# Performance work log

Measured on AMD Instinct MI355X. Metric: run time of the kernel, lower is better.

## Reference

```python
import jax, jax.numpy as jnp
import numpy as np

B, M, S, N, DIN, C = 2048, 5, 128, 128, 64, 32
MID = C // 2  # 16
EPS = 1e-5
NEG_SLOPE = 0.2


def setup_inputs() -> dict:
    key = jax.random.key(0)
    ks = jax.random.split(key, 13)
    sc = lambda fan: 1.0 / np.sqrt(fan)
    return {
        "x_global": jax.random.normal(ks[0], (B, N, C), jnp.float32),
        "x_local": jax.random.normal(ks[1], (B * M, S, DIN), jnp.float32),
        "W_lin": jax.random.normal(ks[2], (C, DIN), jnp.float32) * sc(DIN),
        "b_lin": jnp.zeros((C,), jnp.float32),
        "W_att": jax.random.normal(ks[3], (C,), jnp.float32) * sc(C),  # Conv2d(C,1,1) weight
        "Wa": jax.random.normal(ks[4], (MID, C), jnp.float32) * sc(C),
        "Wb": jax.random.normal(ks[5], (MID, C), jnp.float32) * sc(C),
        "Wc": jax.random.normal(ks[6], (MID, C), jnp.float32) * sc(C),
        "Wn": jax.random.normal(ks[7], (MID, MID), jnp.float32) * sc(MID),
        "Wl": jax.random.normal(ks[8], (MID, MID), jnp.float32) * sc(MID),
        "Wd": jax.random.normal(ks[9], (C, 2 * MID), jnp.float32) * sc(2 * MID),
        "bn_gamma": jnp.ones((C,), jnp.float32),
        "bn_beta": jnp.zeros((C,), jnp.float32),
    }


def reference(x_global, x_local, W_lin, b_lin, W_att, Wa, Wb, Wc, Wn, Wl, Wd, bn_gamma, bn_beta):
    # --- Motion_Aggregation_Module.forward ---
    xl = x_local.reshape(B, M, S, DIN)
    xl = jnp.einsum('bmsd,cd->bmsc', xl, W_lin) + b_lin          # Linear(64,32)
    curves = jnp.transpose(xl, (0, 3, 1, 2))                      # [B,C,M,S]
    x = jnp.transpose(x_global, (0, 2, 1))                        # [B,C,N]

    # --- Correlation_Module.forward ---
    att = jnp.einsum('c,bcms->bms', W_att, curves)                # line_conv_att -> [B,M,S]
    inter = jnp.einsum('bcms,bms->bcm', curves, jax.nn.softmax(att, axis=-1))  # [B,C,M]
    intra = jnp.einsum('bcms,bms->bcs', curves, jax.nn.softmax(att, axis=-2))  # [B,C,S]

    inter = jnp.einsum('oc,bcm->bom', Wa, inter)                  # conva -> [B,MID,M]
    intra = jnp.einsum('oc,bcs->bos', Wb, intra)                  # convb -> [B,MID,S]
    x_logits = jnp.einsum('oc,bcn->bno', Wc, x)                   # convc^T -> [B,N,MID]

    a_inter = jax.nn.softmax(jnp.einsum('bno,bom->bnm', x_logits, inter), axis=-1)  # [B,N,M]
    a_intra = jax.nn.softmax(jnp.einsum('bno,bos->bns', x_logits, intra), axis=-1)  # [B,N,S]

    v_inter = jnp.einsum('po,bom->bmp', Wn, inter)                # convn^T -> [B,M,MID]
    v_intra = jnp.einsum('po,bos->bsp', Wl, intra)                # convl^T -> [B,S,MID]

    f_inter = jnp.einsum('bnm,bmp->bnp', a_inter, v_inter)        # [B,N,MID]
    f_intra = jnp.einsum('bns,bsp->bnp', a_intra, v_intra)        # [B,N,MID]
    feat = jnp.concatenate([f_inter, f_intra], axis=-1)           # [B,N,2*MID]
    feat = jnp.einsum('oc,bnc->bon', Wd, feat)                    # convd conv -> [B,C,N]

    # BatchNorm1d (training mode: batch stats over (B, N), biased variance)
    mean = feat.mean(axis=(0, 2), keepdims=True)
    var = feat.var(axis=(0, 2), keepdims=True)
    feat = (feat - mean) * jax.lax.rsqrt(var + EPS)
    feat = feat * bn_gamma[None, :, None] + bn_beta[None, :, None]

    out = x + feat                                                # residual
    out = jnp.where(out >= 0, out, NEG_SLOPE * out)               # leaky_relu(0.2)
    return jnp.transpose(out, (0, 2, 1))                          # [B,N,C]
```

## Files before the change

### kernel.cpp

```cpp
#include <hip/hip_runtime.h>
#include <math.h>

#define NB 2048
typedef float f32x4 __attribute__((ext_vector_type(4)));

#define P_WAL 0
#define P_WBL 1024
#define P_WLBL 2048
#define P_WNAL 3072
#define P_WEFF 4096
#define P_BWA 4160
#define P_BWB 4176
#define P_BWL 4192
#define P_BWN 4208
#define P_C0  4224

#define WS_BNPART 4352
#define WS_COEF   135424
#define WS_SMALL  135488
#define WS_BIG_I  463168
#define WS_BIG_V  (463168 + 4194304)

#define BSTAGE(MASK, HALF)                                        \
  { const bool hi_ = (lane & (MASK)) != 0;                        \
    _Pragma("unroll")                                             \
    for (int k_ = 0; k_ < (HALF); ++k_) {                         \
      float mine_ = hi_ ? a[k_ + (HALF)] : a[k_];                 \
      float oth_  = hi_ ? a[k_] : a[k_ + (HALF)];                 \
      a[k_] = mine_ + __shfl_xor(oth_, (MASK));                   \
    } }

__global__ __launch_bounds__(256) void k0_pre(const float* __restrict__ W_lin,
                                              const float* __restrict__ b_lin,
                                              const float* __restrict__ W_att,
                                              const float* __restrict__ Wa,
                                              const float* __restrict__ Wb,
                                              const float* __restrict__ Wn,
                                              const float* __restrict__ Wl,
                                              float* __restrict__ pre) {
  int t = threadIdx.x;
  for (int i = t; i < 1024; i += 256) {
    int o = i >> 6, d = i & 63;
    float sa = 0.f, sb = 0.f;
    for (int c = 0; c < 32; ++c) {
      float wl = W_lin[c * 64 + d];
      sa += Wa[o * 32 + c] * wl;
      sb += Wb[o * 32 + c] * wl;
    }
    pre[P_WAL + i] = sa;
    pre[P_WBL + i] = sb;
  }
  if (t < 64) {
    float s = 0.f;
    for (int c = 0; c < 32; ++c) s += W_att[c] * W_lin[c * 64 + t];
    pre[P_WEFF + t] = s;
  }
  if (t < 16) {
    float sa = 0.f, sb = 0.f;
    for (int c = 0; c < 32; ++c) {
      sa += Wa[t * 32 + c] * b_lin[c];
      sb += Wb[t * 32 + c] * b_lin[c];
    }
    pre[P_BWA + t] = sa;
    pre[P_BWB + t] = sb;
  }
  if (t == 0) {
    float s = 0.f;
    for (int c = 0; c < 32; ++c) s += W_att[c] * b_lin[c];
    pre[P_C0] = s;
  }
  __syncthreads();
  for (int i = t; i < 1024; i += 256) {
    int p_ = i >> 6, d = i & 63;
    float sl = 0.f, sn = 0.f;
    for (int o = 0; o < 16; ++o) {
      sl += Wl[p_ * 16 + o] * pre[P_WBL + o * 64 + d];
      sn += Wn[p_ * 16 + o] * pre[P_WAL + o * 64 + d];
    }
    pre[P_WLBL + i] = sl;
    pre[P_WNAL + i] = sn;
  }
  if (t < 16) {
    float sl = 0.f, sn = 0.f;
    for (int o = 0; o < 16; ++o) {
      sl += Wl[t * 16 + o] * pre[P_BWB + o];
      sn += Wn[t * 16 + o] * pre[P_BWA + o];
    }
    pre[P_BWL + t] = sl;
    pre[P_BWN + t] = sn;
  }
}

__global__ __launch_bounds__(512, 1) void k1a(
    const float* __restrict__ xl_all, const float* __restrict__ pre,
    float* __restrict__ p_small, float* __restrict__ bigI,
    float* __restrict__ bigV) {
  __shared__ __align__(16) float xaggi[128 * 68];
  __shared__ f32x4 scratch5[5][8][16];
  __shared__ float pe[5][8];
  __shared__ float xagg_inter[5][64];

  const int t = threadIdx.x;
  const int b = blockIdx.x;
  const int lane = t & 63;
  const int w = t >> 6;
  const int q = lane >> 4;
  const int i16 = lane & 15;

  const float* xl = xl_all + (size_t)b * (5 * 128 * 64);
  const f32x4 weff4 = ((const f32x4*)(pre + P_WEFF))[i16];
  const float c0 = pre[P_C0];

  const float* xb = xl + (size_t)(16 * w + q) * 64 + 4 * i16;

  f32x4 xA[4], xB[4], acc[4];
  float Zk[4];
  #pragma unroll
  for (int k = 0; k < 4; ++k) {
    acc[k] = (f32x4)0.f;
    Zk[k] = 0.f;
    xA[k] = *(const f32x4*)(xb + k * 256);
  }

  #pragma unroll
  for (int m = 0; m < 5; ++m) {
    f32x4* xc = (m & 1) ? xB : xA;
    f32x4* xn = (m & 1) ? xA : xB;
    if (m < 4) {
      const float* np = xb + (size_t)(m + 1) * 8192;
      #pragma unroll
      for (int k = 0; k < 4; ++k) xn[k] = *(const f32x4*)(np + k * 256);
    }
    float a0, a1, a2, a3;
    {
      f32x4 p0 = xc[0] * weff4, p1 = xc[1] * weff4, p2 = xc[2] * weff4, p3 = xc[3] * weff4;
      a0 = p0.x + p0.y + p0.z + p0.w;
      a1 = p1.x + p1.y + p1.z + p1.w;
      a2 = p2.x + p2.y + p2.z + p2.w;
      a3 = p3.x + p3.y + p3.z + p3.w;
    }
    #pragma unroll
    for (int mask = 1; mask <= 8; mask <<= 1) {
      a0 += __shfl_xor(a0, mask);
      a1 += __shfl_xor(a1, mask);
      a2 += __shfl_xor(a2, mask);
      a3 += __shfl_xor(a3, mask);
    }
    float e0 = __expf(a0 + c0), e1 = __expf(a1 + c0);
    float e2 = __expf(a2 + c0), e3 = __expf(a3 + c0);
    Zk[0] += e0; Zk[1] += e1; Zk[2] += e2; Zk[3] += e3;
    f32x4 pim;
    {
      f32x4 pr0 = e0 * xc[0];
      f32x4 pr1 = e1 * xc[1];
      f32x4 pr2 = e2 * xc[2];
      f32x4 pr3 = e3 * xc[3];
      acc[0] += pr0; acc[1] += pr1; acc[2] += pr2; acc[3] += pr3;
      pim = pr0 + pr1 + pr2 + pr3;
    }
    float se = e0 + e1 + e2 + e3;
    #pragma unroll
    for (int mask = 16; mask <= 32; mask <<= 1) {
      pim.x += __shfl_xor(pim.x, mask);
      pim.y += __shfl_xor(pim.y, mask);
      pim.z += __shfl_xor(pim.z, mask);
      pim.w += __shfl_xor(pim.w, mask);
      se += __shfl_xor(se, mask);
    }
    if (lane < 16) {
      scratch5[m][w][i16] = pim;
      if (i16 == 0) pe[m][w] = se;
    }
  }

  #pragma unroll
  for (int k = 0; k < 4; ++k) {
    float invz = 1.f / Zk[k];
    f32x4 v = acc[k] * invz;
    int r = 16 * w + 4 * k + q;
    *(f32x4*)&xaggi[r * 68 + 4 * i16] = v;
  }
  __syncthreads();

  if (t < 320) {
    int mm = t >> 6, d = t & 63;
    const float* sp = (const float*)&scratch5[mm][0][0];
    float s = 0.f;
    #pragma unroll
    for (int j = 0; j < 8; ++j) s += sp[j * 64 + d];
    float sume = pe[mm][0] + pe[mm][1] + pe[mm][2] + pe[mm][3] +
                 pe[mm][4] + pe[mm][5] + pe[mm][6] + pe[mm][7];
    xagg_inter[mm][d] = s / sume;
  }
  __syncthreads();

  {
    const int q2 = __builtin_amdgcn_readfirstlane(t >> 7);
    const int s2 = t & 127;
    const float* Wbase = pre + ((q2 < 2) ? P_WBL : P_WLBL) + (q2 & 1) * 512;
    const float* xrow = &xaggi[s2 * 68];
    float acc2[8];
    #pragma unroll
    for (int r = 0; r < 8; ++r) acc2[r] = 0.f;
    #pragma unroll
    for (int c = 0; c < 64; c += 4) {
      f32x4 xa = *(const f32x4*)(xrow + c);
      #pragma unroll
      for (int r = 0; r < 8; ++r)
        acc2[r] += xa.x * Wbase[r * 64 + c] + xa.y * Wbase[r * 64 + c + 1] +
                   xa.z * Wbase[r * 64 + c + 2] + xa.w * Wbase[r * 64 + c + 3];
    }
    const int bb = ((q2 < 2) ? P_BWB : P_BWL) + (q2 & 1) * 8;
    float* dst = ((q2 < 2) ? bigI : bigV) + (size_t)b * 2048 + s2 * 16 + (q2 & 1) * 8;
    f32x4 o0, o1;
    o0.x = acc2[0] + pre[bb + 0];
    o0.y = acc2[1] + pre[bb + 1];
    o0.z = acc2[2] + pre[bb + 2];
    o0.w = acc2[3] + pre[bb + 3];
    o1.x = acc2[4] + pre[bb + 4];
    o1.y = acc2[5] + pre[bb + 5];
    o1.z = acc2[6] + pre[bb + 6];
    o1.w = acc2[7] + pre[bb + 7];
    *(f32x4*)dst = o0;
    *(f32x4*)(dst + 4) = o1;
  }

  if (t < 160) {
    int o2 = t & 31, mm = t >> 5;
    const float* wr = pre + ((o2 < 16) ? (P_WAL + o2 * 64) : (P_WNAL + (o2 - 16) * 64));
    float p = 0.f;
    #pragma unroll
    for (int d = 0; d < 64; ++d) p += wr[d] * xagg_inter[mm][d];
    p += (o2 < 16) ? pre[P_BWA + o2] : pre[P_BWN + (o2 - 16)];
    float* os = p_small + (size_t)b * 160;
    if (o2 < 16) os[mm * 16 + o2] = p;
    else os[80 + mm * 16 + (o2 - 16)] = p;
  }
}

__global__ __launch_bounds__(128, 1) void k1b(
    const float* __restrict__ xg_all, const float* __restrict__ Wc_g,
    const float* __restrict__ Wd_g, const float* __restrict__ p_small,
    const float* __restrict__ bigI, const float* __restrict__ bigV,
    float* __restrict__ out, float* __restrict__ bn_part) {
  __shared__ f32x4 slabI[128][4];
  __shared__ f32x4 slabV[128][4];
  __shared__ float part1[2][32];
  __shared__ float part2[2][32];

  const int t = threadIdx.x;
  const int b = blockIdx.x;
  const int lane = t & 63;
  const int w = t >> 6;
  const int kmap = ((lane & 1) << 4) | ((lane & 2) << 2) | (lane & 4) |
                   ((lane >> 2) & 2) | ((lane >> 4) & 1);

  const f32x4* gI = (const f32x4*)(bigI + (size_t)b * 2048);
  const f32x4* gV = (const f32x4*)(bigV + (size_t)b * 2048);
  #pragma unroll
  for (int j = 0; j < 4; ++j) {
    ((f32x4*)slabI)[t + 128 * j] = gI[t + 128 * j];
    ((f32x4*)slabV)[t + 128 * j] = gV[t + 128 * j];
  }

  const f32x4* xgr = (const f32x4*)(xg_all + ((size_t)b * 128 + t) * 32);
  f32x4 xv[8];
  #pragma unroll
  for (int j = 0; j < 8; ++j) xv[j] = xgr[j];
  f32x4 xl4[4];
  #pragma unroll
  for (int o4 = 0; o4 < 4; ++o4) {
    f32x4 r;
    #pragma unroll
    for (int jj = 0; jj < 4; ++jj) {
      const int o = o4 * 4 + jj;
      f32x4 s = (f32x4)0.f;
      #pragma unroll
      for (int j = 0; j < 8; ++j) s += xv[j] * *(const f32x4*)(Wc_g + o * 32 + 4 * j);
      r[jj] = s.x + s.y + s.z + s.w;
    }
    xl4[o4] = r;
  }
  __syncthreads();

  float sum = 0.f;
  f32x4 fa[4];
  #pragma unroll
  for (int j = 0; j < 4; ++j) fa[j] = (f32x4)0.f;
  for (int i = 0; i < 128; ++i) {
    f32x4 d4 = xl4[0] * slabI[i][0] + xl4[1] * slabI[i][1] +
               xl4[2] * slabI[i][2] + xl4[3] * slabI[i][3];
    float e = __expf(d4.x + d4.y + d4.z + d4.w);
    sum += e;
    #pragma unroll
    for (int j = 0; j < 4; ++j) fa[j] += e * slabV[i][j];
  }
  const float inv = 1.f / sum;
  f32x4 fin[4];
  #pragma unroll
  for (int j = 0; j < 4; ++j) fin[j] = fa[j] * inv;

  const float* sm = p_small + (size_t)b * 160;
  float L[5], mx3 = -1e30f;
  #pragma unroll
  for (int mm = 0; mm < 5; ++mm) {
    float p = 0.f;
    #pragma unroll
    for (int o4 = 0; o4 < 4; ++o4) {
      #pragma unroll
      for (int jj = 0; jj < 4; ++jj) p += xl4[o4][jj] * sm[mm * 16 + o4 * 4 + jj];
    }
    L[mm] = p;
    mx3 = fmaxf(mx3, p);
  }
  float sum3 = 0.f;
  #pragma unroll
  for (int mm = 0; mm < 5; ++mm) { L[mm] = __expf(L[mm] - mx3); sum3 += L[mm]; }
  const float inv3 = 1.f / sum3;
  f32x4 fi[4];
  #pragma unroll
  for (int o4 = 0; o4 < 4; ++o4) {
    f32x4 r;
    #pragma unroll
    for (int jj = 0; jj < 4; ++jj) {
      float p = 0.f;
      #pragma unroll
      for (int mm = 0; mm < 5; ++mm) p += L[mm] * sm[80 + mm * 16 + o4 * 4 + jj];
      r[jj] = p * inv3;
    }
    fi[o4] = r;
  }

  f32x4 feat[8];
  #pragma unroll
  for (int o4 = 0; o4 < 8; ++o4) {
    f32x4 r;
    #pragma unroll
    for (int jj = 0; jj < 4; ++jj) {
      const int o = o4 * 4 + jj;
      f32x4 s = (f32x4)0.f;
      #pragma unroll
      for (int j = 0; j < 4; ++j) {
        s += fi[j]  * *(const f32x4*)(Wd_g + o * 32 + 4 * j);
        s += fin[j] * *(const f32x4*)(Wd_g + o * 32 + 16 + 4 * j);
      }
      r[jj] = s.x + s.y + s.z + s.w;
    }
    feat[o4] = r;
  }
  f32x4* op = (f32x4*)(out + ((size_t)b * 128 + t) * 32);
  #pragma unroll
  for (int o4 = 0; o4 < 8; ++o4) op[o4] = feat[o4];

  {
    float a[32];
    #pragma unroll
    for (int o = 0; o < 32; ++o) a[o] = feat[o >> 2][o & 3];
    BSTAGE(1, 16) BSTAGE(2, 8) BSTAGE(4, 4) BSTAGE(8, 2) BSTAGE(16, 1)
    a[0] += __shfl_xor(a[0], 32);
    if (lane < 32) part1[w][kmap] = a[0];
  }
  {
    float a[32];
    #pragma unroll
    for (int o = 0; o < 32; ++o) { float v = feat[o >> 2][o & 3]; a[o] = v * v; }
    BSTAGE(1, 16) BSTAGE(2, 8) BSTAGE(4, 4) BSTAGE(8, 2) BSTAGE(16, 1)
    a[0] += __shfl_xor(a[0], 32);
    if (lane < 32) part2[w][kmap] = a[0];
  }
  __syncthreads();
  if (t < 64) {
    int c = t & 31, h = t >> 5;
    float v = h ? (part2[0][c] + part2[1][c]) : (part1[0][c] + part1[1][c]);
    bn_part[(size_t)b * 64 + h * 32 + c] = v;
  }
}

__global__ __launch_bounds__(256, 1) void k2_stats(const float* __restrict__ bn_part,
                                                   const float* __restrict__ gamma,
                                                   const float* __restrict__ beta,
                                                   float* __restrict__ coef) {
  __shared__ float red[2][4];
  const int c = blockIdx.x;
  const int t = threadIdx.x;
  const int lane = t & 63, w = t >> 6;
  float s1 = 0.f, s2 = 0.f;
  for (int bb = t; bb < NB; bb += 256) {
    s1 += bn_part[(size_t)bb * 64 + c];
    s2 += bn_part[(size_t)bb * 64 + c + 32];
  }
  #pragma unroll
  for (int mask = 1; mask <= 32; mask <<= 1) {
    s1 += __shfl_xor(s1, mask);
    s2 += __shfl_xor(s2, mask);
  }
  if (lane == 0) { red[0][w] = s1; red[1][w] = s2; }
  __syncthreads();
  if (t == 0) {
    float S1 = red[0][0] + red[0][1] + red[0][2] + red[0][3];
    float S2 = red[1][0] + red[1][1] + red[1][2] + red[1][3];
    const float inv = 1.f / (float)(NB * 128);
    float mean = S1 * inv;
    float var = S2 * inv - mean * mean;
    float scl = gamma[c] * rsqrtf(var + 1e-5f);
    coef[c] = scl;
    coef[32 + c] = beta[c] - mean * scl;
  }
}

__global__ __launch_bounds__(256) void k3_final(const float* __restrict__ xg,
                                                float* __restrict__ out,
                                                const float* __restrict__ coef) {
  __shared__ float s_c[64];
  if (threadIdx.x < 64) s_c[threadIdx.x] = coef[threadIdx.x];
  __syncthreads();
  size_t i4 = (size_t)blockIdx.x * 256 + threadIdx.x;
  float4 f = ((const float4*)out)[i4];
  float4 x = ((const float4*)xg)[i4];
  int c = (int)((i4 * 4) & 31);
  float4 r;
  r.x = x.x + f.x * s_c[c + 0] + s_c[32 + c + 0];
  r.y = x.y + f.y * s_c[c + 1] + s_c[32 + c + 1];
  r.z = x.z + f.z * s_c[c + 2] + s_c[32 + c + 2];
  r.w = x.w + f.w * s_c[c + 3] + s_c[32 + c + 3];
  r.x = r.x >= 0.f ? r.x : 0.2f * r.x;
  r.y = r.y >= 0.f ? r.y : 0.2f * r.y;
  r.z = r.z >= 0.f ? r.z : 0.2f * r.z;
  r.w = r.w >= 0.f ? r.w : 0.2f * r.w;
  ((float4*)out)[i4] = r;
}

extern "C" void kernel_launch(void* const* d_in, const int* in_sizes, int n_in,
                              void* d_out, int out_size, void* d_ws, size_t ws_size,
                              hipStream_t stream) {
  const float* xg    = (const float*)d_in[0];
  const float* xl    = (const float*)d_in[1];
  const float* W_lin = (const float*)d_in[2];
  const float* b_lin = (const float*)d_in[3];
  const float* W_att = (const float*)d_in[4];
  const float* Wa    = (const float*)d_in[5];
  const float* Wb    = (const float*)d_in[6];
  const float* Wc    = (const float*)d_in[7];
  const float* Wn    = (const float*)d_in[8];
  const float* Wl    = (const float*)d_in[9];
  const float* Wd    = (const float*)d_in[10];
  const float* gamma = (const float*)d_in[11];
  const float* beta  = (const float*)d_in[12];
  float* out = (float*)d_out;
  float* ws = (float*)d_ws;
  float* pre = ws;
  float* bn_part = ws + WS_BNPART;
  float* coef = ws + WS_COEF;
  float* p_small = ws + WS_SMALL;
  float* bigI = ws + WS_BIG_I;
  float* bigV = ws + WS_BIG_V;

  hipLaunchKernelGGL(k0_pre, dim3(1), dim3(256), 0, stream,
                     W_lin, b_lin, W_att, Wa, Wb, Wn, Wl, pre);
  hipLaunchKernelGGL(k1a, dim3(NB), dim3(512), 0, stream, xl, pre, p_small, bigI, bigV);
  hipLaunchKernelGGL(k1b, dim3(NB), dim3(128), 0, stream,
                     xg, Wc, Wd, p_small, bigI, bigV, out, bn_part);
  hipLaunchKernelGGL(k2_stats, dim3(32), dim3(256), 0, stream, bn_part, gamma, beta, coef);
  hipLaunchKernelGGL(k3_final, dim3(8192), dim3(256), 0, stream, xg, out, coef);
}
```

Before: 197.2 us.

## Fuse k1a and k1b into one kernel keeping intermediates in LDS

Merges the two per-batch kernels into a single 512-thread block, so the per-sample intra/value slabs and small inter vectors stay in shared memory instead of round-tripping through global workspace. The 128-step intra attention loop is split across four thread groups of 32 steps each and combined through a reused shared buffer, and the inner products switch to float2 vectors. Launch bounds are raised to allow two blocks per CU. The cost is more LDS per block, an extra barrier and combine step, and only 128 of the 512 threads doing the final projection and BN partials.

```diff
diff --git a/kernel.cpp b/kernel.cpp
--- a/kernel.cpp
+++ b/kernel.cpp
@@ -3,6 +3,7 @@
 
 #define NB 2048
 typedef float f32x4 __attribute__((ext_vector_type(4)));
+typedef float f32x2 __attribute__((ext_vector_type(2)));
 
 #define P_WAL 0
 #define P_WBL 1024
@@ -17,9 +18,6 @@
 
 #define WS_BNPART 4352
 #define WS_COEF   135424
-#define WS_SMALL  135488
-#define WS_BIG_I  463168
-#define WS_BIG_V  (463168 + 4194304)
 
 #define BSTAGE(MASK, HALF)                                        \
   { const bool hi_ = (lane & (MASK)) != 0;                        \
@@ -91,14 +89,22 @@
   }
 }
 
-__global__ __launch_bounds__(512, 1) void k1a(
-    const float* __restrict__ xl_all, const float* __restrict__ pre,
-    float* __restrict__ p_small, float* __restrict__ bigI,
-    float* __restrict__ bigV) {
-  __shared__ __align__(16) float xaggi[128 * 68];
-  __shared__ f32x4 scratch5[5][8][16];
-  __shared__ float pe[5][8];
-  __shared__ float xagg_inter[5][64];
+__global__ __launch_bounds__(512, 2) void k1_fused(
+    const float* __restrict__ xl_all, const float* __restrict__ xg_all,
+    const float* __restrict__ pre, const float* __restrict__ Wc_g,
+    const float* __restrict__ Wd_g, float* __restrict__ out,
+    float* __restrict__ bn_part) {
+  __shared__ __align__(16) char R1[46592];
+  float* xaggi = (float*)R1;
+  f32x4 (*scratch5)[8][16] = (f32x4(*)[8][16])(R1 + 34816);
+  float* pe = (float*)(R1 + 45056);
+  float* xagg_inter = (float*)(R1 + 45216);
+  float (*comb)[19] = (float(*)[19])R1;
+  __shared__ f32x4 slabI[128][4];
+  __shared__ f32x4 slabV[128][4];
+  __shared__ float s_small[160];
+  __shared__ float part1[2][32];
+  __shared__ float part2[2][32];
 
   const int t = threadIdx.x;
   const int b = blockIdx.x;
@@ -112,7 +118,6 @@
   const float c0 = pre[P_C0];
 
   const float* xb = xl + (size_t)(16 * w + q) * 64 + 4 * i16;
-
   f32x4 xA[4], xB[4], acc[4];
   float Zk[4];
   #pragma unroll
@@ -121,7 +126,6 @@
     Zk[k] = 0.f;
     xA[k] = *(const f32x4*)(xb + k * 256);
   }
-
   #pragma unroll
   for (int m = 0; m < 5; ++m) {
     f32x4* xc = (m & 1) ? xB : xA;
@@ -169,10 +173,9 @@
     }
     if (lane < 16) {
       scratch5[m][w][i16] = pim;
-      if (i16 == 0) pe[m][w] = se;
-    }
-  }
-
+      if (i16 == 0) pe[m * 8 + w] = se;
+    }
+  }
   #pragma unroll
   for (int k = 0; k < 4; ++k) {
     float invz = 1.f / Zk[k];
@@ -188,9 +191,9 @@
     float s = 0.f;
     #pragma unroll
     for (int j = 0; j < 8; ++j) s += sp[j * 64 + d];
-    float sume = pe[mm][0] + pe[mm][1] + pe[mm][2] + pe[mm][3] +
-                 pe[mm][4] + pe[mm][5] + pe[mm][6] + pe[mm][7];
-    xagg_inter[mm][d] = s / sume;
+    float sume = pe[mm * 8 + 0] + pe[mm * 8 + 1] + pe[mm * 8 + 2] + pe[mm * 8 + 3] +
+                 pe[mm * 8 + 4] + pe[mm * 8 + 5] + pe[mm * 8 + 6] + pe[mm * 8 + 7];
+    xagg_inter[mm * 64 + d] = s / sume;
   }
   __syncthreads();
 
@@ -198,175 +201,161 @@
     const int q2 = __builtin_amdgcn_readfirstlane(t >> 7);
     const int s2 = t & 127;
     const float* Wbase = pre + ((q2 < 2) ? P_WBL : P_WLBL) + (q2 & 1) * 512;
-    const float* xrow = &xaggi[s2 * 68];
-    float acc2[8];
-    #pragma unroll
-    for (int r = 0; r < 8; ++r) acc2[r] = 0.f;
-    #pragma unroll
-    for (int c = 0; c < 64; c += 4) {
-      f32x4 xa = *(const f32x4*)(xrow + c);
+    const f32x2* xrow2 = (const f32x2*)&xaggi[s2 * 68];
+    f32x2 a2[8];
+    #pragma unroll
+    for (int r = 0; r < 8; ++r) a2[r] = (f32x2)0.f;
+    #pragma unroll
+    for (int c2 = 0; c2 < 32; ++c2) {
+      f32x2 xa = xrow2[c2];
       #pragma unroll
       for (int r = 0; r < 8; ++r)
-        acc2[r] += xa.x * Wbase[r * 64 + c] + xa.y * Wbase[r * 64 + c + 1] +
-                   xa.z * Wbase[r * 64 + c + 2] + xa.w * Wbase[r * 64 + c + 3];
+        a2[r] += xa * *(const f32x2*)(Wbase + r * 64 + 2 * c2);
     }
     const int bb = ((q2 < 2) ? P_BWB : P_BWL) + (q2 & 1) * 8;
-    float* dst = ((q2 < 2) ? bigI : bigV) + (size_t)b * 2048 + s2 * 16 + (q2 & 1) * 8;
+    f32x4* dst = ((q2 < 2) ? &slabI[s2][0] : &slabV[s2][0]) + (q2 & 1) * 2;
     f32x4 o0, o1;
-    o0.x = acc2[0] + pre[bb + 0];
-    o0.y = acc2[1] + pre[bb + 1];
-    o0.z = acc2[2] + pre[bb + 2];
-    o0.w = acc2[3] + pre[bb + 3];
-    o1.x = acc2[4] + pre[bb + 4];
-    o1.y = acc2[5] + pre[bb + 5];
-    o1.z = acc2[6] + pre[bb + 6];
-    o1.w = acc2[7] + pre[bb + 7];
-    *(f32x4*)dst = o0;
-    *(f32x4*)(dst + 4) = o1;
-  }
-
+    o0.x = a2[0].x + a2[0].y + pre[bb + 0];
+    o0.y = a2[1].x + a2[1].y + pre[bb + 1];
+    o0.z = a2[2].x + a2[2].y + pre[bb + 2];
+    o0.w = a2[3].x + a2[3].y + pre[bb + 3];
+    o1.x = a2[4].x + a2[4].y + pre[bb + 4];
+    o1.y = a2[5].x + a2[5].y + pre[bb + 5];
+    o1.z = a2[6].x + a2[6].y + pre[bb + 6];
+    o1.w = a2[7].x + a2[7].y + pre[bb + 7];
+    dst[0] = o0;
+    dst[1] = o1;
+  }
   if (t < 160) {
     int o2 = t & 31, mm = t >> 5;
     const float* wr = pre + ((o2 < 16) ? (P_WAL + o2 * 64) : (P_WNAL + (o2 - 16) * 64));
     float p = 0.f;
     #pragma unroll
-    for (int d = 0; d < 64; ++d) p += wr[d] * xagg_inter[mm][d];
+    for (int d = 0; d < 64; ++d) p += wr[d] * xagg_inter[mm * 64 + d];
     p += (o2 < 16) ? pre[P_BWA + o2] : pre[P_BWN + (o2 - 16)];
-    float* os = p_small + (size_t)b * 160;
-    if (o2 < 16) os[mm * 16 + o2] = p;
-    else os[80 + mm * 16 + (o2 - 16)] = p;
-  }
-}
-
-__global__ __launch_bounds__(128, 1) void k1b(
-    const float* __restrict__ xg_all, const float* __restrict__ Wc_g,
-    const float* __restrict__ Wd_g, const float* __restrict__ p_small,
-    const float* __restrict__ bigI, const float* __restrict__ bigV,
-    float* __restrict__ out, float* __restrict__ bn_part) {
-  __shared__ f32x4 slabI[128][4];
-  __shared__ f32x4 slabV[128][4];
-  __shared__ float part1[2][32];
-  __shared__ float part2[2][32];
-
-  const int t = threadIdx.x;
-  const int b = blockIdx.x;
-  const int lane = t & 63;
-  const int w = t >> 6;
-  const int kmap = ((lane & 1) << 4) | ((lane & 2) << 2) | (lane & 4) |
-                   ((lane >> 2) & 2) | ((lane >> 4) & 1);
-
-  const f32x4* gI = (const f32x4*)(bigI + (size_t)b * 2048);
-  const f32x4* gV = (const f32x4*)(bigV + (size_t)b * 2048);
-  #pragma unroll
-  for (int j = 0; j < 4; ++j) {
-    ((f32x4*)slabI)[t + 128 * j] = gI[t + 128 * j];
-    ((f32x4*)slabV)[t + 128 * j] = gV[t + 128 * j];
-  }
-
-  const f32x4* xgr = (const f32x4*)(xg_all + ((size_t)b * 128 + t) * 32);
-  f32x4 xv[8];
-  #pragma unroll
-  for (int j = 0; j < 8; ++j) xv[j] = xgr[j];
-  f32x4 xl4[4];
-  #pragma unroll
-  for (int o4 = 0; o4 < 4; ++o4) {
-    f32x4 r;
-    #pragma unroll
-    for (int jj = 0; jj < 4; ++jj) {
-      const int o = o4 * 4 + jj;
-      f32x4 s = (f32x4)0.f;
-      #pragma unroll
-      for (int j = 0; j < 8; ++j) s += xv[j] * *(const f32x4*)(Wc_g + o * 32 + 4 * j);
-      r[jj] = s.x + s.y + s.z + s.w;
-    }
-    xl4[o4] = r;
-  }
-  __syncthreads();
-
-  float sum = 0.f;
-  f32x4 fa[4];
-  #pragma unroll
-  for (int j = 0; j < 4; ++j) fa[j] = (f32x4)0.f;
-  for (int i = 0; i < 128; ++i) {
-    f32x4 d4 = xl4[0] * slabI[i][0] + xl4[1] * slabI[i][1] +
-               xl4[2] * slabI[i][2] + xl4[3] * slabI[i][3];
-    float e = __expf(d4.x + d4.y + d4.z + d4.w);
-    sum += e;
-    #pragma unroll
-    for (int j = 0; j < 4; ++j) fa[j] += e * slabV[i][j];
-  }
-  const float inv = 1.f / sum;
-  f32x4 fin[4];
-  #pragma unroll
-  for (int j = 0; j < 4; ++j) fin[j] = fa[j] * inv;
-
-  const float* sm = p_small + (size_t)b * 160;
-  float L[5], mx3 = -1e30f;
-  #pragma unroll
-  for (int mm = 0; mm < 5; ++mm) {
-    float p = 0.f;
-    #pragma unroll
-    for (int o4 = 0; o4 < 4; ++o4) {
-      #pragma unroll
-      for (int jj = 0; jj < 4; ++jj) p += xl4[o4][jj] * sm[mm * 16 + o4 * 4 + jj];
-    }
-    L[mm] = p;
-    mx3 = fmaxf(mx3, p);
-  }
-  float sum3 = 0.f;
-  #pragma unroll
-  for (int mm = 0; mm < 5; ++mm) { L[mm] = __expf(L[mm] - mx3); sum3 += L[mm]; }
-  const float inv3 = 1.f / sum3;
-  f32x4 fi[4];
-  #pragma unroll
-  for (int o4 = 0; o4 < 4; ++o4) {
-    f32x4 r;
-    #pragma unroll
-    for (int jj = 0; jj < 4; ++jj) {
+    if (o2 < 16) s_small[mm * 16 + o2] = p;
+    else s_small[80 + mm * 16 + (o2 - 16)] = p;
+  }
+
+  const int n = t & 127;
+  f32x2 xl2[8];
+  {
+    const f32x2* xgr = (const f32x2*)(xg_all + ((size_t)b * 128 + n) * 32);
+    f32x2 xv[16];
+    #pragma unroll
+    for (int j = 0; j < 16; ++j) xv[j] = xgr[j];
+    #pragma unroll
+    for (int o2 = 0; o2 < 8; ++o2) {
+      f32x2 r;
+      #pragma unroll
+      for (int jj = 0; jj < 2; ++jj) {
+        const int o = o2 * 2 + jj;
+        f32x2 s = (f32x2)0.f;
+        #pragma unroll
+        for (int j = 0; j < 16; ++j) s += xv[j] * *(const f32x2*)(Wc_g + o * 32 + 2 * j);
+        r[jj] = s.x + s.y;
+      }
+      xl2[o2] = r;
+    }
+  }
+  __syncthreads();
+
+  {
+    const int j4 = t >> 7;
+    float sum = 0.f;
+    f32x2 fa2[8];
+    #pragma unroll
+    for (int j = 0; j < 8; ++j) fa2[j] = (f32x2)0.f;
+    for (int i = 32 * j4; i < 32 * j4 + 32; ++i) {
+      const f32x2* sI = (const f32x2*)&slabI[i][0];
+      f32x2 d2 = xl2[0] * sI[0];
+      #pragma unroll
+      for (int j = 1; j < 8; ++j) d2 += xl2[j] * sI[j];
+      float e = __expf(d2.x + d2.y);
+      sum += e;
+      f32x2 e2; e2.x = e; e2.y = e;
+      const f32x2* sV = (const f32x2*)&slabV[i][0];
+      #pragma unroll
+      for (int j = 0; j < 8; ++j) fa2[j] += e2 * sV[j];
+    }
+    comb[t][0] = sum;
+    #pragma unroll
+    for (int j = 0; j < 8; ++j) { comb[t][1 + 2 * j] = fa2[j].x; comb[t][2 + 2 * j] = fa2[j].y; }
+  }
+  __syncthreads();
+
+  float fo[32];
+  if (t < 128) {
+    float tot = comb[n][0] + comb[n + 128][0] + comb[n + 256][0] + comb[n + 384][0];
+    float inv = 1.f / tot;
+    f32x2 fin2[8];
+    #pragma unroll
+    for (int j = 0; j < 8; ++j) {
+      fin2[j].x = (comb[n][1 + 2 * j] + comb[n + 128][1 + 2 * j] +
+                   comb[n + 256][1 + 2 * j] + comb[n + 384][1 + 2 * j]) * inv;
+      fin2[j].y = (comb[n][2 + 2 * j] + comb[n + 128][2 + 2 * j] +
+                   comb[n + 256][2 + 2 * j] + comb[n + 384][2 + 2 * j]) * inv;
+    }
+    float L[5], mx3 = -1e30f;
+    #pragma unroll
+    for (int mm = 0; mm < 5; ++mm) {
       float p = 0.f;
       #pragma unroll
-      for (int mm = 0; mm < 5; ++mm) p += L[mm] * sm[80 + mm * 16 + o4 * 4 + jj];
-      r[jj] = p * inv3;
-    }
-    fi[o4] = r;
-  }
-
-  f32x4 feat[8];
-  #pragma unroll
-  for (int o4 = 0; o4 < 8; ++o4) {
-    f32x4 r;
-    #pragma unroll
-    for (int jj = 0; jj < 4; ++jj) {
-      const int o = o4 * 4 + jj;
-      f32x4 s = (f32x4)0.f;
-      #pragma unroll
-      for (int j = 0; j < 4; ++j) {
-        s += fi[j]  * *(const f32x4*)(Wd_g + o * 32 + 4 * j);
-        s += fin[j] * *(const f32x4*)(Wd_g + o * 32 + 16 + 4 * j);
+      for (int j = 0; j < 8; ++j) {
+        p += xl2[j].x * s_small[mm * 16 + 2 * j];
+        p += xl2[j].y * s_small[mm * 16 + 2 * j + 1];
       }
-      r[jj] = s.x + s.y + s.z + s.w;
-    }
-    feat[o4] = r;
-  }
-  f32x4* op = (f32x4*)(out + ((size_t)b * 128 + t) * 32);
-  #pragma unroll
-  for (int o4 = 0; o4 < 8; ++o4) op[o4] = feat[o4];
-
-  {
-    float a[32];
-    #pragma unroll
-    for (int o = 0; o < 32; ++o) a[o] = feat[o >> 2][o & 3];
-    BSTAGE(1, 16) BSTAGE(2, 8) BSTAGE(4, 4) BSTAGE(8, 2) BSTAGE(16, 1)
-    a[0] += __shfl_xor(a[0], 32);
-    if (lane < 32) part1[w][kmap] = a[0];
-  }
-  {
-    float a[32];
-    #pragma unroll
-    for (int o = 0; o < 32; ++o) { float v = feat[o >> 2][o & 3]; a[o] = v * v; }
-    BSTAGE(1, 16) BSTAGE(2, 8) BSTAGE(4, 4) BSTAGE(8, 2) BSTAGE(16, 1)
-    a[0] += __shfl_xor(a[0], 32);
-    if (lane < 32) part2[w][kmap] = a[0];
+      L[mm] = p;
+      mx3 = fmaxf(mx3, p);
+    }
+    float sum3 = 0.f;
+    #pragma unroll
+    for (int mm = 0; mm < 5; ++mm) { L[mm] = __expf(L[mm] - mx3); sum3 += L[mm]; }
+    const float inv3 = 1.f / sum3;
+    f32x2 fi2[8];
+    #pragma unroll
+    for (int j = 0; j < 8; ++j) {
+      f32x2 r = (f32x2)0.f;
+      #pragma unroll
+      for (int mm = 0; mm < 5; ++mm) {
+        r.x += L[mm] * s_small[80 + mm * 16 + 2 * j];
+        r.y += L[mm] * s_small[80 + mm * 16 + 2 * j + 1];
+      }
+      fi2[j].x = r.x * inv3;
+      fi2[j].y = r.y * inv3;
+    }
+    #pragma unroll
+    for (int o = 0; o < 32; ++o) {
+      const f32x2* wd = (const f32x2*)(Wd_g + o * 32);
+      f32x2 s = fi2[0] * wd[0];
+      #pragma unroll
+      for (int j = 1; j < 8; ++j) s += fi2[j] * wd[j];
+      #pragma unroll
+      for (int j = 0; j < 8; ++j) s += fin2[j] * wd[8 + j];
+      fo[o] = s.x + s.y;
+    }
+    float* op = out + ((size_t)b * 128 + n) * 32;
+    #pragma unroll
+    for (int o4 = 0; o4 < 8; ++o4)
+      ((f32x4*)op)[o4] = *(f32x4*)&fo[4 * o4];
+    const int kmap = ((lane & 1) << 4) | ((lane & 2) << 2) | (lane & 4) |
+                     ((lane >> 2) & 2) | ((lane >> 4) & 1);
+    {
+      float a[32];
+      #pragma unroll
+      for (int o = 0; o < 32; ++o) a[o] = fo[o];
+      BSTAGE(1, 16) BSTAGE(2, 8) BSTAGE(4, 4) BSTAGE(8, 2) BSTAGE(16, 1)
+      a[0] += __shfl_xor(a[0], 32);
+      if (lane < 32) part1[w][kmap] = a[0];
+    }
+    {
+      float a[32];
+      #pragma unroll
+      for (int o = 0; o < 32; ++o) a[o] = fo[o] * fo[o];
+      BSTAGE(1, 16) BSTAGE(2, 8) BSTAGE(4, 4) BSTAGE(8, 2) BSTAGE(16, 1)
+      a[0] += __shfl_xor(a[0], 32);
+      if (lane < 32) part2[w][kmap] = a[0];
+    }
   }
   __syncthreads();
   if (t < 64) {
@@ -451,15 +440,11 @@
   float* pre = ws;
   float* bn_part = ws + WS_BNPART;
   float* coef = ws + WS_COEF;
-  float* p_small = ws + WS_SMALL;
-  float* bigI = ws + WS_BIG_I;
-  float* bigV = ws + WS_BIG_V;
 
   hipLaunchKernelGGL(k0_pre, dim3(1), dim3(256), 0, stream,
                      W_lin, b_lin, W_att, Wa, Wb, Wn, Wl, pre);
-  hipLaunchKernelGGL(k1a, dim3(NB), dim3(512), 0, stream, xl, pre, p_small, bigI, bigV);
-  hipLaunchKernelGGL(k1b, dim3(NB), dim3(128), 0, stream,
-                     xg, Wc, Wd, p_small, bigI, bigV, out, bn_part);
+  hipLaunchKernelGGL(k1_fused, dim3(NB), dim3(512), 0, stream,
+                     xl, xg, pre, Wc, Wd, out, bn_part);
   hipLaunchKernelGGL(k2_stats, dim3(32), dim3(256), 0, stream, bn_part, gamma, beta, coef);
   hipLaunchKernelGGL(k3_final, dim3(8192), dim3(256), 0, stream, xg, out, coef);
 }
```

Result: slower. 227.4 us (+15.3%).
